# Performance work log

Hardware: AMD Instinct MI355X
Metric: run time of the kernel (lower is better)

The kernel has to match this reference:

```python
import jax, jax.numpy as jnp
import numpy as np

N, D = 4096, 1024

def setup_inputs() -> dict:
    key = jax.random.key(0)
    ks = jax.random.split(key, 7)
    s = 1.0 / np.sqrt(D)
    return {
        "x": jax.random.normal(ks[0], (N, D), dtype=jnp.float32),
        "Wq": jax.random.uniform(ks[1], (D, D), jnp.float32, -s, s),
        "bq": jax.random.uniform(ks[2], (D,), jnp.float32, -s, s),
        "Wk": jax.random.uniform(ks[3], (D, D), jnp.float32, -s, s),
        "bk": jax.random.uniform(ks[4], (D,), jnp.float32, -s, s),
        "Wv": jax.random.uniform(ks[5], (D, D), jnp.float32, -s, s),
        "bv": jax.random.uniform(ks[6], (D,), jnp.float32, -s, s),
    }

def reference(x, Wq, bq, Wk, bk, Wv, bv):
    # Linear layers: y = x @ W^T + b (torch convention, W is [out, in]; here square)
    Q = x @ Wq.T + bq  # [N, D]
    K = x @ Wk.T + bk  # [N, D]
    V = x @ Wv.T + bv  # [N, D]
    scores = (Q @ K.T) / jnp.sqrt(jnp.asarray(x.shape[-1], x.dtype))  # [N, N]
    attn = jax.nn.softmax(scores, axis=-1)
    return attn @ V  # [N, D]
```

## Files before the change

kernel.cpp:

```cpp
#include <hip/hip_runtime.h>


#define N_TOK 4096
#define DDIM  1024

typedef short s16x4 __attribute__((ext_vector_type(4)));
typedef short s16x8 __attribute__((ext_vector_type(8)));
typedef float f32x4 __attribute__((ext_vector_type(4)));

#define VMCNT0() asm volatile("s_waitcnt vmcnt(0)" ::: "memory")
#define VMCNT6() asm volatile("s_waitcnt vmcnt(6)" ::: "memory")
#define VMCNT8() asm volatile("s_waitcnt vmcnt(8)" ::: "memory")
#define LGKMCNT0() asm volatile("s_waitcnt lgkmcnt(0)" ::: "memory")
#define BARRIER() do { asm volatile("" ::: "memory"); \
                       __builtin_amdgcn_s_barrier();  \
                       asm volatile("" ::: "memory"); } while (0)

__device__ inline short f2b(float f) {
  unsigned int u = __float_as_uint(f);
  unsigned int r = (u + 0x7FFFu + ((u >> 16) & 1u)) >> 16;
  return (short)(unsigned short)r;
}

__device__ __forceinline__ void gld_lds16(const short* g, short* l) {
  __builtin_amdgcn_global_load_lds(
      (const __attribute__((address_space(1))) unsigned int*)g,
      (__attribute__((address_space(3))) unsigned int*)l, 16, 0, 0);
}

__device__ __forceinline__ void xcd_remap(int gx, int& bx, int& by) {
  const int L = by * gx + bx;
  const int g = L & 7, h = L >> 3;
  by = g * 4 + (h & 3);
  bx = h >> 2;
}

template<int MODE>
__device__ __forceinline__ void gemm_pipe128(
    const short* __restrict__ A, const short* __restrict__ B,
    void* __restrict__ C, const float* __restrict__ aux,
    short (*smem)[(128 + 128) * 64],
    int K, int ld, int ldc, float scale, int row0, int col0)
{
  constexpr int BM = 128, BN = 128, BK = 64;
  const int NT = K / BK;

  const int tid  = threadIdx.x;
  const int wave = tid >> 6, lane = tid & 63;
  const int wm = wave >> 1, wn = wave & 1;
  const int quad = lane >> 4, lr = lane & 15;

  auto stage = [&](int t, int sl) {
    #pragma unroll
    for (int c = 0; c < 8; c++) {
      const int id = c * 256 + tid;
      const int r  = id >> 3;
      const int q  = (id & 7) ^ (r & 7);
      const short* src = (r < BM)
          ? A + (size_t)(row0 + r) * ld + t * BK + q * 8
          : B + (size_t)(col0 + r - BM) * ld + t * BK + q * 8;
      gld_lds16(src, &smem[sl][(c * 256 + wave * 64) * 8]);
    }
  };

  f32x4 acc[4][4];
  #pragma unroll
  for (int i = 0; i < 4; i++)
    #pragma unroll
    for (int j = 0; j < 4; j++) acc[i][j] = {0.f, 0.f, 0.f, 0.f};

  stage(0, 0);
  stage(1, 1);
  VMCNT8();
  BARRIER();

  for (int t = 0; t < NT; t++) {
    const int sl = t & 1;
    const short* As = smem[sl];
    const short* Bs = smem[sl] + BM * BK;

    s16x8 af[2][4], bf[2][4];
    #pragma unroll
    for (int h = 0; h < 2; h++) {
      #pragma unroll
      for (int i = 0; i < 4; i++) {
        const int row = wm * 64 + i * 16 + lr;
        const int ch = (h * 4 + quad) ^ (row & 7);
        af[h][i] = *reinterpret_cast<const s16x8*>(&As[(row * 8 + ch) * 8]);
      }
      #pragma unroll
      for (int j = 0; j < 4; j++) {
        const int row = wn * 64 + j * 16 + lr;
        const int ch = (h * 4 + quad) ^ (row & 7);
        bf[h][j] = *reinterpret_cast<const s16x8*>(&Bs[(row * 8 + ch) * 8]);
      }
    }
    LGKMCNT0();
    __builtin_amdgcn_sched_barrier(0);
    BARRIER();

    const bool pf = (t + 2) < NT;
    if (pf) stage(t + 2, sl);

    __builtin_amdgcn_s_setprio(1);
    #pragma unroll
    for (int h = 0; h < 2; h++)
      #pragma unroll
      for (int i = 0; i < 4; i++)
        #pragma unroll
        for (int j = 0; j < 4; j++)
          acc[i][j] = __builtin_amdgcn_mfma_f32_16x16x32_bf16(
              af[h][i], bf[h][j], acc[i][j], 0, 0, 0);
    __builtin_amdgcn_s_setprio(0);

    if (pf) { VMCNT8(); } else { VMCNT0(); }
    BARRIER();
  }

  if constexpr (MODE == 0) {
    float bb[4];
    #pragma unroll
    for (int j = 0; j < 4; j++) bb[j] = aux[col0 + wn * 64 + j * 16 + lr];
    #pragma unroll
    for (int i = 0; i < 4; i++) {
      const int r0 = row0 + wm * 64 + i * 16 + quad * 4;
      #pragma unroll
      for (int j = 0; j < 4; j++) {
        const int c = col0 + wn * 64 + j * 16 + lr;
        #pragma unroll
        for (int r = 0; r < 4; r++)
          ((short*)C)[(size_t)(r0 + r) * ldc + c] = f2b(acc[i][j][r] * scale + bb[j]);
      }
    }
  } else {
    float bb[4];
    #pragma unroll
    for (int j = 0; j < 4; j++) bb[j] = aux[col0 + wn * 64 + j * 16 + lr];
    short* trans = &smem[0][0];
    #pragma unroll
    for (int i = 0; i < 4; i++) {
      const int rl = wm * 64 + i * 16 + quad * 4;
      #pragma unroll
      for (int j = 0; j < 4; j++) {
        const int cl = wn * 64 + j * 16 + lr;
        s16x4 v;
        #pragma unroll
        for (int r = 0; r < 4; r++) v[r] = f2b(acc[i][j][r] * scale + bb[j]);
        *reinterpret_cast<s16x4*>(&trans[cl * 136 + rl]) = v;
      }
    }
    BARRIER();
    #pragma unroll
    for (int s = 0; s < 8; s++) {
      const int u = s * 256 + tid;
      const int cc = u >> 4;
      const int seg = u & 15;
      s16x8 v = *reinterpret_cast<const s16x8*>(&trans[cc * 136 + seg * 8]);
      *reinterpret_cast<s16x8*>(
          &((short*)C)[(size_t)(col0 + cc) * ldc + row0 + seg * 8]) = v;
    }
  }
}

#define XU  (N_TOK * DDIM / 8)
#define WU  (DDIM * DDIM / 8)
#define NCVT ((XU + 3 * WU) / 256)
__global__ __launch_bounds__(256)
void cvt_all(const float* __restrict__ x,  const float* __restrict__ wq,
             const float* __restrict__ wk, const float* __restrict__ wv,
             short* __restrict__ xb, short* __restrict__ wqb,
             short* __restrict__ wkb, short* __restrict__ wvb,
             float* __restrict__ rowsum)
{
  if (blockIdx.x >= NCVT) {
    float4 z = {0.f, 0.f, 0.f, 0.f};
    float4* p = reinterpret_cast<float4*>(rowsum) + threadIdx.x * 4;
    p[0] = z; p[1] = z; p[2] = z; p[3] = z;
    return;
  }
  int gid = blockIdx.x * 256 + threadIdx.x;
  const float* src; short* dst; int off;
  if (gid < XU)               { src = x;  dst = xb;  off = gid; }
  else if (gid < XU + WU)     { src = wq; dst = wqb; off = gid - XU; }
  else if (gid < XU + 2 * WU) { src = wk; dst = wkb; off = gid - XU - WU; }
  else                        { src = wv; dst = wvb; off = gid - XU - 2 * WU; }
  const float4* g = reinterpret_cast<const float4*>(src) + (size_t)off * 2;
  float4 a = g[0], b = g[1];
  s16x8 o;
  o[0] = f2b(a.x); o[1] = f2b(a.y); o[2] = f2b(a.z); o[3] = f2b(a.w);
  o[4] = f2b(b.x); o[5] = f2b(b.y); o[6] = f2b(b.z); o[7] = f2b(b.w);
  reinterpret_cast<s16x8*>(dst)[off] = o;
}

__global__ __launch_bounds__(256, 2)
void k_qkv(const short* __restrict__ xb,
           const short* __restrict__ Wqb, const short* __restrict__ Wkb,
           const short* __restrict__ Wvb,
           const float* __restrict__ bq, const float* __restrict__ bk,
           const float* __restrict__ bv,
           short* __restrict__ Qb, short* __restrict__ Kb, short* __restrict__ Vt)
{
  __shared__ short smem[2][(128 + 128) * 64];
  int bx = blockIdx.x, by = blockIdx.y;
  xcd_remap(DDIM / 128, bx, by);
  if (blockIdx.z == 0) {
    gemm_pipe128<0>(xb, Wqb, Qb, bq, smem, DDIM, DDIM, DDIM,
                    1.0f, by * 128, bx * 128);
  } else if (blockIdx.z == 1) {
    gemm_pipe128<0>(xb, Wkb, Kb, bk, smem, DDIM, DDIM, DDIM,
                    1.0f, by * 128, bx * 128);
  } else {
    gemm_pipe128<3>(xb, Wvb, Vt, bv, smem, DDIM, DDIM, N_TOK,
                    1.0f, by * 128, bx * 128);
  }
}

__global__ __launch_bounds__(256, 2)
void k_score(const short* __restrict__ Qb, const short* __restrict__ Kb,
             short* __restrict__ SP, float* __restrict__ rowsum)
{
  constexpr int BM = 128, BN = 128, BK = 64;
  constexpr int NT = DDIM / BK;
  __shared__ short smem[2][(BM + BN) * BK];

  int bx = blockIdx.x, by = blockIdx.y;
  xcd_remap(32, bx, by);
  const int row0 = by * BM, col0 = bx * BN;

  const int tid  = threadIdx.x;
  const int wave = tid >> 6, lane = tid & 63;
  const int wm = wave >> 1, wn = wave & 1;
  const int quad = lane >> 4, lr = lane & 15;

  auto stage = [&](int t, int sl) {
    #pragma unroll
    for (int c = 0; c < 8; c++) {
      const int id = c * 256 + tid;
      const int r  = id >> 3;
      const int q  = (id & 7) ^ (r & 7);
      const short* src = (r < BM)
          ? Qb + (size_t)(row0 + r) * DDIM + t * BK + q * 8
          : Kb + (size_t)(col0 + r - BM) * DDIM + t * BK + q * 8;
      gld_lds16(src, &smem[sl][(c * 256 + wave * 64) * 8]);
    }
  };

  f32x4 acc[4][4];
  #pragma unroll
  for (int i = 0; i < 4; i++)
    #pragma unroll
    for (int j = 0; j < 4; j++) acc[i][j] = {0.f, 0.f, 0.f, 0.f};

  stage(0, 0);
  stage(1, 1);
  VMCNT8();
  BARRIER();

  for (int t = 0; t < NT; t++) {
    const int sl = t & 1;
    const short* As = smem[sl];
    const short* Bs = smem[sl] + BM * BK;

    s16x8 af[2][4], bf[2][4];
    #pragma unroll
    for (int h = 0; h < 2; h++) {
      #pragma unroll
      for (int i = 0; i < 4; i++) {
        const int row = wm * 64 + i * 16 + lr;
        const int ch = (h * 4 + quad) ^ (row & 7);
        af[h][i] = *reinterpret_cast<const s16x8*>(&As[(row * 8 + ch) * 8]);
      }
      #pragma unroll
      for (int j = 0; j < 4; j++) {
        const int row = wn * 64 + j * 16 + lr;
        const int ch = (h * 4 + quad) ^ (row & 7);
        bf[h][j] = *reinterpret_cast<const s16x8*>(&Bs[(row * 8 + ch) * 8]);
      }
    }
    LGKMCNT0();
    __builtin_amdgcn_sched_barrier(0);
    BARRIER();

    const bool pf = (t + 2) < NT;
    if (pf) stage(t + 2, sl);

    __builtin_amdgcn_s_setprio(1);
    #pragma unroll
    for (int h = 0; h < 2; h++)
      #pragma unroll
      for (int i = 0; i < 4; i++)
        #pragma unroll
        for (int j = 0; j < 4; j++)
          acc[i][j] = __builtin_amdgcn_mfma_f32_16x16x32_bf16(
              af[h][i], bf[h][j], acc[i][j], 0, 0, 0);
    __builtin_amdgcn_s_setprio(0);

    if (pf) { VMCNT8(); } else { VMCNT0(); }
    BARRIER();
  }

  constexpr float scale = 0.03125f;
  #pragma unroll
  for (int i = 0; i < 4; i++) {
    const int r0 = row0 + wm * 64 + i * 16 + quad * 4;
    float ex[4][4];
    #pragma unroll
    for (int j = 0; j < 4; j++) {
      const int c = col0 + wn * 64 + j * 16 + lr;
      #pragma unroll
      for (int r = 0; r < 4; r++) {
        ex[j][r] = __expf(acc[i][j][r] * scale);
        SP[(size_t)(r0 + r) * N_TOK + c] = f2b(ex[j][r]);
      }
    }
    #pragma unroll
    for (int r = 0; r < 4; r++) {
      float s = 0.f;
      #pragma unroll
      for (int j = 0; j < 4; j++) s += ex[j][r];
      s += __shfl_xor(s, 1, 64);
      s += __shfl_xor(s, 2, 64);
      s += __shfl_xor(s, 4, 64);
      s += __shfl_xor(s, 8, 64);
      if (lr == 0) atomicAdd(&rowsum[r0 + r], s);
    }
  }
}

__global__ __launch_bounds__(256, 2)
void k_pv(const short* __restrict__ SP, const short* __restrict__ Vt,
          float* __restrict__ out, const float* __restrict__ rowsum)
{
  constexpr int BM = 128, BN = 64, BK = 64;
  constexpr int NT = N_TOK / BK;
  __shared__ short smem[2][(BM + BN) * BK];

  int bx = blockIdx.x, by = blockIdx.y;
  xcd_remap(DDIM / 64, bx, by);
  const int row0 = by * BM, col0 = bx * BN;

  const int tid  = threadIdx.x;
  const int wave = tid >> 6, lane = tid & 63;
  const int wm = wave >> 1, wn = wave & 1;
  const int quad = lane >> 4, lr = lane & 15;

  auto stage = [&](int t, int sl) {
    #pragma unroll
    for (int c = 0; c < 6; c++) {
      const int id = c * 256 + tid;
      const int r  = id >> 3;
      const int q  = (id & 7) ^ (r & 7);
      const short* src = (r < BM)
          ? SP + (size_t)(row0 + r) * N_TOK + t * BK + q * 8
          : Vt + (size_t)(col0 + r - BM) * N_TOK + t * BK + q * 8;
      gld_lds16(src, &smem[sl][(c * 256 + wave * 64) * 8]);
    }
  };

  f32x4 acc[4][2];
  #pragma unroll
  for (int i = 0; i < 4; i++)
    #pragma unroll
    for (int j = 0; j < 2; j++) acc[i][j] = {0.f, 0.f, 0.f, 0.f};

  stage(0, 0);
  stage(1, 1);
  VMCNT6();
  BARRIER();

  for (int t = 0; t < NT; t++) {
    const int sl = t & 1;
    const short* As = smem[sl];
    const short* Bs = smem[sl] + BM * BK;

    s16x8 af[2][4], bf[2][2];
    #pragma unroll
    for (int h = 0; h < 2; h++) {
      #pragma unroll
      for (int i = 0; i < 4; i++) {
        const int row = wm * 64 + i * 16 + lr;
        const int ch = (h * 4 + quad) ^ (row & 7);
        af[h][i] = *reinterpret_cast<const s16x8*>(&As[(row * 8 + ch) * 8]);
      }
      #pragma unroll
      for (int j = 0; j < 2; j++) {
        const int row = wn * 32 + j * 16 + lr;
        const int ch = (h * 4 + quad) ^ (row & 7);
        bf[h][j] = *reinterpret_cast<const s16x8*>(&Bs[(row * 8 + ch) * 8]);
      }
    }
    LGKMCNT0();
    __builtin_amdgcn_sched_barrier(0);
    BARRIER();

    const bool pf = (t + 2) < NT;
    if (pf) stage(t + 2, sl);

    __builtin_amdgcn_s_setprio(1);
    #pragma unroll
    for (int h = 0; h < 2; h++)
      #pragma unroll
      for (int i = 0; i < 4; i++)
        #pragma unroll
        for (int j = 0; j < 2; j++)
          acc[i][j] = __builtin_amdgcn_mfma_f32_16x16x32_bf16(
              af[h][i], bf[h][j], acc[i][j], 0, 0, 0);
    __builtin_amdgcn_s_setprio(0);

    if (pf) { VMCNT6(); } else { VMCNT0(); }
    BARRIER();
  }

  #pragma unroll
  for (int i = 0; i < 4; i++) {
    const int r0 = row0 + wm * 64 + i * 16 + quad * 4;
    float linv[4];
    #pragma unroll
    for (int r = 0; r < 4; r++) linv[r] = 1.0f / rowsum[r0 + r];
    #pragma unroll
    for (int j = 0; j < 2; j++) {
      const int c = col0 + wn * 32 + j * 16 + lr;
      #pragma unroll
      for (int r = 0; r < 4; r++)
        out[(size_t)(r0 + r) * DDIM + c] = acc[i][j][r] * linv[r];
    }
  }
}

extern "C" void kernel_launch(void* const* d_in, const int* in_sizes, int n_in,
                              void* d_out, int out_size, void* d_ws, size_t ws_size,
                              hipStream_t stream)
{
  const float* x  = (const float*)d_in[0];
  const float* Wq = (const float*)d_in[1];
  const float* bq = (const float*)d_in[2];
  const float* Wk = (const float*)d_in[3];
  const float* bk = (const float*)d_in[4];
  const float* Wv = (const float*)d_in[5];
  const float* bv = (const float*)d_in[6];
  float* out = (float*)d_out;

  char* ws = (char*)d_ws;
  const size_t MB = 1024 * 1024;
  short* Qb  = (short*)(ws + 0 * MB);
  short* Kb  = (short*)(ws + 8 * MB);
  short* Vt  = (short*)(ws + 24 * MB);
  short* SP  = (short*)(ws + 32 * MB);
  short* xb  = (short*)(ws + 32 * MB);
  short* Wqb = (short*)(ws + 40 * MB);
  short* Wkb = (short*)(ws + 42 * MB);
  short* Wvb = (short*)(ws + 44 * MB);
  float* rowsum = (float*)(ws + 64 * MB);

  dim3 b256(256);

  cvt_all<<<dim3(NCVT + 1), b256, 0, stream>>>(
      x, Wq, Wk, Wv, xb, Wqb, Wkb, Wvb, rowsum);

  k_qkv<<<dim3(DDIM / 128, N_TOK / 128, 3), b256, 0, stream>>>(
      xb, Wqb, Wkb, Wvb, bq, bk, bv, Qb, Kb, Vt);

  k_score<<<dim3(32, 32), b256, 0, stream>>>(Qb, Kb, SP, rowsum);

  k_pv<<<dim3(DDIM / 64, N_TOK / 128), b256, 0, stream>>>(
      SP, Vt, out, rowsum);
}
```

Before: 197.7 us.

## Enlarge score kernel tile to 256x256 with 8 waves and quadrant-interleaved pipeline

The Q·K^T score kernel moves from 128x128 tiles with 4 waves to 256x256 tiles with 8 waves (512 threads). Each wave now computes a 128x64 sub-tile in four quadrant MFMA phases, and global-to-LDS loads are staged in half-tile pieces between the phases. The aim is more operand reuse per byte loaded and better overlap of loads with MFMA work. In exchange it uses 128KB of LDS, more accumulator registers, many more barriers, and launches only 256 blocks, which may leave some CUs underused.

```diff
diff --git a/kernel.cpp b/kernel.cpp
--- a/kernel.cpp
+++ b/kernel.cpp
@@ -9,9 +9,11 @@
 typedef float f32x4 __attribute__((ext_vector_type(4)));
 
 #define VMCNT0() asm volatile("s_waitcnt vmcnt(0)" ::: "memory")
+#define VMCNT4() asm volatile("s_waitcnt vmcnt(4)" ::: "memory")
 #define VMCNT6() asm volatile("s_waitcnt vmcnt(6)" ::: "memory")
 #define VMCNT8() asm volatile("s_waitcnt vmcnt(8)" ::: "memory")
 #define LGKMCNT0() asm volatile("s_waitcnt lgkmcnt(0)" ::: "memory")
+#define SCHEDB() __builtin_amdgcn_sched_barrier(0)
 #define BARRIER() do { asm volatile("" ::: "memory"); \
                        __builtin_amdgcn_s_barrier();  \
                        asm volatile("" ::: "memory"); } while (0)
@@ -33,6 +35,12 @@
   const int g = L & 7, h = L >> 3;
   by = g * 4 + (h & 3);
   bx = h >> 2;
+}
+__device__ __forceinline__ void xcd_remap16(int gx, int& bx, int& by) {
+  const int L = by * gx + bx;
+  const int g = L & 7, h = L >> 3;
+  by = g * 2 + (h & 1);
+  bx = h >> 1;
 }
 
 template<int MODE>
@@ -96,7 +104,7 @@
       }
     }
     LGKMCNT0();
-    __builtin_amdgcn_sched_barrier(0);
+    SCHEDB();
     BARRIER();
 
     const bool pf = (t + 2) < NT;
@@ -215,94 +223,139 @@
   }
 }
 
-__global__ __launch_bounds__(256, 2)
+#define READ_AF(As, MH) do {                                                  \
+    _Pragma("unroll")                                                         \
+    for (int kh = 0; kh < 2; kh++)                                            \
+      _Pragma("unroll")                                                       \
+      for (int f = 0; f < 4; f++) {                                           \
+        const int row_ = wm * 128 + (MH) * 64 + f * 16 + lr;                  \
+        const int ch_ = (kh * 4 + quad) ^ (row_ & 7);                         \
+        af[kh][f] = *reinterpret_cast<const s16x8*>(&(As)[(row_ * 8 + ch_) * 8]); \
+      }                                                                       \
+  } while (0)
+
+#define READ_BF(Bs, NH, BF) do {                                              \
+    _Pragma("unroll")                                                         \
+    for (int kh = 0; kh < 2; kh++)                                            \
+      _Pragma("unroll")                                                       \
+      for (int g = 0; g < 2; g++) {                                           \
+        const int row_ = wn * 64 + (NH) * 32 + g * 16 + lr;                   \
+        const int ch_ = (kh * 4 + quad) ^ (row_ & 7);                         \
+        BF[kh][g] = *reinterpret_cast<const s16x8*>(&(Bs)[(row_ * 8 + ch_) * 8]); \
+      }                                                                       \
+  } while (0)
+
+#define MFMA_Q(MH, NH, BF) do {                                               \
+    __builtin_amdgcn_s_setprio(1);                                            \
+    _Pragma("unroll")                                                         \
+    for (int kh = 0; kh < 2; kh++)                                            \
+      _Pragma("unroll")                                                       \
+      for (int f = 0; f < 4; f++)                                             \
+        _Pragma("unroll")                                                     \
+        for (int g = 0; g < 2; g++)                                           \
+          acc[(MH) * 4 + f][(NH) * 2 + g] =                                   \
+              __builtin_amdgcn_mfma_f32_16x16x32_bf16(                        \
+                  af[kh][f], BF[kh][g], acc[(MH) * 4 + f][(NH) * 2 + g],      \
+                  0, 0, 0);                                                   \
+    __builtin_amdgcn_s_setprio(0);                                            \
+  } while (0)
+
+__global__ __launch_bounds__(512, 2)
 void k_score(const short* __restrict__ Qb, const short* __restrict__ Kb,
              short* __restrict__ SP, float* __restrict__ rowsum)
 {
-  constexpr int BM = 128, BN = 128, BK = 64;
-  constexpr int NT = DDIM / BK;
-  __shared__ short smem[2][(BM + BN) * BK];
+  constexpr int NITER = 8;
+  __shared__ short smem[2][32768];
 
   int bx = blockIdx.x, by = blockIdx.y;
-  xcd_remap(32, bx, by);
-  const int row0 = by * BM, col0 = bx * BN;
+  xcd_remap16(16, bx, by);
+  const int row0 = by * 256, col0 = bx * 256;
 
   const int tid  = threadIdx.x;
   const int wave = tid >> 6, lane = tid & 63;
-  const int wm = wave >> 1, wn = wave & 1;
+  const int wm = wave >> 2, wn = wave & 3;
   const int quad = lane >> 4, lr = lane & 15;
 
-  auto stage = [&](int t, int sl) {
-    #pragma unroll
-    for (int c = 0; c < 8; c++) {
-      const int id = c * 256 + tid;
+  auto stage_h = [&](int t, int b, int h) {
+    const short* gbase = (h < 2)
+        ? Qb + (size_t)(row0 + (h & 1) * 128) * DDIM
+        : Kb + (size_t)(col0 + (h & 1) * 128) * DDIM;
+    short* dst = &smem[b][(h >> 1) * 16384 + (h & 1) * 8192];
+    #pragma unroll
+    for (int c = 0; c < 2; c++) {
+      const int id = c * 512 + tid;
       const int r  = id >> 3;
       const int q  = (id & 7) ^ (r & 7);
-      const short* src = (r < BM)
-          ? Qb + (size_t)(row0 + r) * DDIM + t * BK + q * 8
-          : Kb + (size_t)(col0 + r - BM) * DDIM + t * BK + q * 8;
-      gld_lds16(src, &smem[sl][(c * 256 + wave * 64) * 8]);
+      gld_lds16(gbase + (size_t)r * DDIM + t * 64 + q * 8,
+                dst + (c * 512 + wave * 64) * 8);
     }
   };
 
-  f32x4 acc[4][4];
+  s16x8 af[2][4], bf0[2][2], bf1[2][2];
+  f32x4 acc[8][4];
   #pragma unroll
-  for (int i = 0; i < 4; i++)
+  for (int i = 0; i < 8; i++)
     #pragma unroll
     for (int j = 0; j < 4; j++) acc[i][j] = {0.f, 0.f, 0.f, 0.f};
 
-  stage(0, 0);
-  stage(1, 1);
-  VMCNT8();
+  const short* As0 = smem[0];
+  const short* Bs0 = smem[0] + 16384;
+  const short* As1 = smem[1];
+  const short* Bs1 = smem[1] + 16384;
+
+  stage_h(0, 0, 2); stage_h(0, 0, 3); stage_h(0, 0, 0); stage_h(0, 0, 1);
+  stage_h(1, 1, 2); stage_h(1, 1, 0);
+  VMCNT4();
   BARRIER();
 
-  for (int t = 0; t < NT; t++) {
-    const int sl = t & 1;
-    const short* As = smem[sl];
-    const short* Bs = smem[sl] + BM * BK;
-
-    s16x8 af[2][4], bf[2][4];
-    #pragma unroll
-    for (int h = 0; h < 2; h++) {
-      #pragma unroll
-      for (int i = 0; i < 4; i++) {
-        const int row = wm * 64 + i * 16 + lr;
-        const int ch = (h * 4 + quad) ^ (row & 7);
-        af[h][i] = *reinterpret_cast<const s16x8*>(&As[(row * 8 + ch) * 8]);
-      }
-      #pragma unroll
-      for (int j = 0; j < 4; j++) {
-        const int row = wn * 64 + j * 16 + lr;
-        const int ch = (h * 4 + quad) ^ (row & 7);
-        bf[h][j] = *reinterpret_cast<const s16x8*>(&Bs[(row * 8 + ch) * 8]);
-      }
-    }
-    LGKMCNT0();
-    __builtin_amdgcn_sched_barrier(0);
-    BARRIER();
-
-    const bool pf = (t + 2) < NT;
-    if (pf) stage(t + 2, sl);
-
-    __builtin_amdgcn_s_setprio(1);
-    #pragma unroll
-    for (int h = 0; h < 2; h++)
-      #pragma unroll
-      for (int i = 0; i < 4; i++)
-        #pragma unroll
-        for (int j = 0; j < 4; j++)
-          acc[i][j] = __builtin_amdgcn_mfma_f32_16x16x32_bf16(
-              af[h][i], bf[h][j], acc[i][j], 0, 0, 0);
-    __builtin_amdgcn_s_setprio(0);
-
-    if (pf) { VMCNT8(); } else { VMCNT0(); }
+  for (int i = 0; i < NITER; i++) {
+    const int t1 = 2 * i + 1;
+    const bool more = (i + 1) < NITER;
+
+    READ_AF(As0, 0); READ_BF(Bs0, 0, bf0);
+    stage_h(t1, 1, 3);
+    BARRIER(); LGKMCNT0(); SCHEDB();
+    MFMA_Q(0, 0, bf0);
+    BARRIER();
+    READ_BF(Bs0, 1, bf1);
+    stage_h(t1, 1, 1);
+    BARRIER(); LGKMCNT0(); SCHEDB();
+    MFMA_Q(0, 1, bf1);
+    BARRIER();
+    READ_AF(As0, 1);
+    if (more) stage_h(t1 + 1, 0, 2);
+    BARRIER(); LGKMCNT0(); SCHEDB();
+    MFMA_Q(1, 1, bf1);
+    BARRIER();
+    if (more) { stage_h(t1 + 1, 0, 0); VMCNT4(); } else { VMCNT0(); }
+    BARRIER();
+    MFMA_Q(1, 0, bf0);
+    BARRIER();
+    READ_AF(As1, 0); READ_BF(Bs1, 0, bf0);
+    if (more) stage_h(t1 + 1, 0, 3);
+    BARRIER(); LGKMCNT0(); SCHEDB();
+    MFMA_Q(0, 0, bf0);
+    BARRIER();
+    READ_BF(Bs1, 1, bf1);
+    if (more) stage_h(t1 + 1, 0, 1);
+    BARRIER(); LGKMCNT0(); SCHEDB();
+    MFMA_Q(0, 1, bf1);
+    BARRIER();
+    READ_AF(As1, 1);
+    if (more) stage_h(t1 + 2, 1, 2);
+    BARRIER(); LGKMCNT0(); SCHEDB();
+    MFMA_Q(1, 1, bf1);
+    BARRIER();
+    if (more) { stage_h(t1 + 2, 1, 0); VMCNT4(); } else { VMCNT0(); }
+    BARRIER();
+    MFMA_Q(1, 0, bf0);
     BARRIER();
   }
 
   constexpr float scale = 0.03125f;
   #pragma unroll
-  for (int i = 0; i < 4; i++) {
-    const int r0 = row0 + wm * 64 + i * 16 + quad * 4;
+  for (int i = 0; i < 8; i++) {
+    const int r0 = row0 + wm * 128 + i * 16 + quad * 4;
     float ex[4][4];
     #pragma unroll
     for (int j = 0; j < 4; j++) {
@@ -390,7 +443,7 @@
       }
     }
     LGKMCNT0();
-    __builtin_amdgcn_sched_barrier(0);
+    SCHEDB();
     BARRIER();
 
     const bool pf = (t + 2) < NT;
@@ -460,7 +513,7 @@
   k_qkv<<<dim3(DDIM / 128, N_TOK / 128, 3), b256, 0, stream>>>(
       xb, Wqb, Wkb, Wvb, bq, bk, bv, Qb, Kb, Vt);
 
-  k_score<<<dim3(32, 32), b256, 0, stream>>>(Qb, Kb, SP, rowsum);
+  k_score<<<dim3(16, 16), dim3(512), 0, stream>>>(Qb, Kb, SP, rowsum);
 
   k_pv<<<dim3(DDIM / 64, N_TOK / 128), b256, 0, stream>>>(
       SP, Vt, out, rowsum);
```

Result: no change. 196.8 us (-0.5%).
